# Optimization experiments

Hardware: AMD Instinct MI355X
Metric: run time of the kernel (lower is better)

## Reference

```python
import jax, jax.numpy as jnp
import numpy as np

B, T, C, I = 4, 4096, 1024, 4096

def rmsnorm(x, w, eps=1e-6):
    return x * jax.lax.rsqrt(jnp.mean(x * x, axis=-1, keepdims=True) + eps) * w

def shift(h):
    # prepend zeros, drop last timestep: (B,T,C)
    return jnp.pad(h, ((0, 0), (1, 0), (0, 0)))[:, :-1]

def wkv_scan(k, v, w, u):
    # k, v: (B,T,C) fp32; w, u: (C,)
    ew = jnp.exp(jnp.clip(w, -20.0, 20.0))
    def step(carry, kv):
        a, b = carry
        kt, vt = kv  # (B,C)
        ekt = jnp.exp(jnp.clip(u + kt, -20.0, 20.0))
        out = (a + ekt * vt) / (b + ekt + 1e-8)
        ek = jnp.exp(jnp.clip(kt, -20.0, 20.0))
        return (ew * a + ek * vt, ew * b + ek), out
    init = (jnp.zeros((k.shape[0], k.shape[2]), jnp.float32),
            jnp.zeros((k.shape[0], k.shape[2]), jnp.float32))
    _, out = jax.lax.scan(step, init, (k.swapaxes(0, 1), v.swapaxes(0, 1)))
    return out.swapaxes(0, 1)  # (B,T,C)

def setup_inputs() -> dict:
    key = jax.random.key(0)
    ks = jax.random.split(key, 16)
    s = 1.0 / np.sqrt(C)
    si = 1.0 / np.sqrt(I)
    return {
        "x": jax.random.normal(ks[0], (B, T, C), jnp.float32),
        "ln1_w": jnp.ones((C,), jnp.float32),
        "ln2_w": jnp.ones((C,), jnp.float32),
        "time_decay": jax.random.normal(ks[1], (C,), jnp.float32) * 0.1 - 5.0,
        "time_first": jax.random.normal(ks[2], (C,), jnp.float32) * 0.01,
        "time_mix_k": jnp.full((C,), 0.5, jnp.float32),
        "time_mix_v": jnp.full((C,), 0.5, jnp.float32),
        "time_mix_r": jnp.full((C,), 0.5, jnp.float32),
        "W_key": jax.random.normal(ks[3], (C, C), jnp.float32) * s,
        "W_value": jax.random.normal(ks[4], (C, C), jnp.float32) * s,
        "W_recept": jax.random.normal(ks[5], (C, C), jnp.float32) * s,
        "W_out": jax.random.normal(ks[6], (C, C), jnp.float32) * s,
        "time_mix_k2": jnp.full((C,), 0.5, jnp.float32),
        "time_mix_r2": jnp.full((C,), 0.5, jnp.float32),
        "W_key2": jax.random.normal(ks[7], (C, I), jnp.float32) * s,
        "W_value2": jax.random.normal(ks[8], (I, C), jnp.float32) * si,
        "W_recept2": jax.random.normal(ks[9], (C, C), jnp.float32) * s,
    }

def reference(x, ln1_w, ln2_w, time_decay, time_first,
              time_mix_k, time_mix_v, time_mix_r,
              W_key, W_value, W_recept, W_out,
              time_mix_k2, time_mix_r2, W_key2, W_value2, W_recept2):
    # --- time mixing ---
    h = rmsnorm(x, ln1_w)
    sh = shift(h)
    xk = h * time_mix_k + sh * (1 - time_mix_k)
    xv = h * time_mix_v + sh * (1 - time_mix_v)
    xr = h * time_mix_r + sh * (1 - time_mix_r)
    k = xk @ W_key
    v = xv @ W_value
    r = jax.nn.sigmoid(xr @ W_recept)
    w = -jnp.exp(time_decay)
    u = time_first
    wkv = wkv_scan(k.astype(jnp.float32), v.astype(jnp.float32), w, u).astype(x.dtype)
    x = x + (r * wkv) @ W_out
    # --- channel mixing ---
    h = rmsnorm(x, ln2_w)
    sh = shift(h)
    xk = h * time_mix_k2 + sh * (1 - time_mix_k2)
    xr = h * time_mix_r2 + sh * (1 - time_mix_r2)
    k2 = jnp.square(jax.nn.relu(xk @ W_key2))
    r2 = jax.nn.sigmoid(xr @ W_recept2)
    return x + r2 * (k2 @ W_value2)
```

## Files before the change

### kernel.cpp

```cpp
#include <hip/hip_runtime.h>
#include <cstdint>
#include <cstddef>

#define B_ 4
#define T_ 4096
#define C_ 1024
#define I_ 4096
#define M_ (B_*T_)

__device__ __forceinline__ float bf2f(uint16_t u) {
    union { uint32_t i; float f; } v; v.i = ((uint32_t)u) << 16; return v.f;
}
__device__ __forceinline__ uint16_t f2bf(float f) {
    union { float f; uint32_t i; } v; v.f = f;
    uint32_t i = v.i;
    return (uint16_t)((i + 0x7fffu + ((i >> 16) & 1u)) >> 16);
}

typedef __bf16 bf16x8 __attribute__((ext_vector_type(8)));
typedef float  f32x4  __attribute__((ext_vector_type(4)));

__device__ __forceinline__ void async16(const void* g, void* l) {
    __builtin_amdgcn_global_load_lds(
        (const __attribute__((address_space(1))) void*)g,
        (__attribute__((address_space(3))) void*)l, 16, 0, 0);
}

__global__ void sniff_kernel(const uint32_t* __restrict__ w,
                             int* __restrict__ flag, int* __restrict__ one) {
    *flag = (w[0] == 0x3F003F00u) ? 1 : 0;
    *one = 1;
}

struct VecPtrs { const void* s[9]; uint16_t* d[9]; };
__global__ __launch_bounds__(256) void convert_vecs(VecPtrs p, const int* __restrict__ flagp) {
    const int f = *flagp;
    const int tid = threadIdx.x;
    for (int a = 0; a < 9; ++a) {
        const void* s = p.s[a]; uint16_t* d = p.d[a];
        for (int i = tid; i < C_; i += 256)
            d[i] = f ? ((const uint16_t*)s)[i] : f2bf(((const float*)s)[i]);
    }
}

struct TJobs { const void* src[7]; uint16_t* dst[7]; };
__global__ __launch_bounds__(256) void transpose_all(TJobs tj, const int* __restrict__ flagp)
{
    __shared__ uint16_t tile[64][65];
    const int f = *flagp;
    const int bid = blockIdx.x;
    int w, t, R, Cc, cx, cy;
    if (bid < 1280) {
        w = bid >> 8; t = bid & 255; R = C_; Cc = C_; cx = t & 15; cy = t >> 4;
    } else if (bid < 2304) {
        w = 5; t = bid - 1280; R = C_; Cc = I_; cx = t & 63; cy = t >> 6;
    } else {
        w = 6; t = bid - 2304; R = I_; Cc = C_; cx = t & 15; cy = t >> 4;
    }
    const void* in = tj.src[w];
    uint16_t* out = tj.dst[w];
    const int lc = threadIdx.x & 63;
    const int rg = threadIdx.x >> 6;
    const int c0 = cx * 64, r0 = cy * 64;
    #pragma unroll
    for (int i = 0; i < 16; ++i) {
        int lr = rg * 16 + i;
        size_t idx = (size_t)(r0 + lr) * Cc + c0 + lc;
        tile[lr][lc] = f ? ((const uint16_t*)in)[idx] : f2bf(((const float*)in)[idx]);
    }
    __syncthreads();
    #pragma unroll
    for (int i = 0; i < 16; ++i) {
        int lcc = rg * 16 + i;
        out[(size_t)(c0 + lcc) * R + r0 + lc] = tile[lc][lcc];
    }
}

__global__ __launch_bounds__(256) void mix_kernel(
    const void* __restrict__ x, const uint16_t* __restrict__ ln,
    const uint16_t* __restrict__ mk, const uint16_t* __restrict__ mv,
    const uint16_t* __restrict__ mr, const int* __restrict__ flagp,
    uint16_t* __restrict__ xk, uint16_t* __restrict__ xv, uint16_t* __restrict__ xr)
{
    const int row = blockIdx.x;
    const int tid = threadIdx.x;
    const int f = *flagp;
    const bool hasPrev = (row & (T_ - 1)) != 0;
    const size_t base = (size_t)row * C_;

    float c[4], p[4];
    if (f) {
        const uint16_t* xb = (const uint16_t*)x;
        uint2 cu = ((const uint2*)(xb + base))[tid];
        uint2 pu; pu.x = 0u; pu.y = 0u;
        if (hasPrev) pu = ((const uint2*)(xb + base - C_))[tid];
        c[0] = bf2f((uint16_t)(cu.x & 0xffff)); c[1] = bf2f((uint16_t)(cu.x >> 16));
        c[2] = bf2f((uint16_t)(cu.y & 0xffff)); c[3] = bf2f((uint16_t)(cu.y >> 16));
        p[0] = bf2f((uint16_t)(pu.x & 0xffff)); p[1] = bf2f((uint16_t)(pu.x >> 16));
        p[2] = bf2f((uint16_t)(pu.y & 0xffff)); p[3] = bf2f((uint16_t)(pu.y >> 16));
    } else {
        const float* xf = (const float*)x;
        float4 cf = ((const float4*)(xf + base))[tid];
        float4 pf; pf.x = pf.y = pf.z = pf.w = 0.f;
        if (hasPrev) pf = ((const float4*)(xf + base - C_))[tid];
        c[0] = cf.x; c[1] = cf.y; c[2] = cf.z; c[3] = cf.w;
        p[0] = pf.x; p[1] = pf.y; p[2] = pf.z; p[3] = pf.w;
    }

    float s1 = c[0]*c[0] + c[1]*c[1] + c[2]*c[2] + c[3]*c[3];
    float s2 = p[0]*p[0] + p[1]*p[1] + p[2]*p[2] + p[3]*p[3];
    #pragma unroll
    for (int off = 32; off > 0; off >>= 1) {
        s1 += __shfl_down(s1, off);
        s2 += __shfl_down(s2, off);
    }
    __shared__ float red[8];
    const int lane = tid & 63, wave = tid >> 6;
    if (lane == 0) { red[wave * 2] = s1; red[wave * 2 + 1] = s2; }
    __syncthreads();
    s1 = red[0] + red[2] + red[4] + red[6];
    s2 = red[1] + red[3] + red[5] + red[7];
    const float rs1 = rsqrtf(s1 * (1.f / C_) + 1e-6f);
    const float rs2 = rsqrtf(s2 * (1.f / C_) + 1e-6f);

    uint2 lnu = ((const uint2*)ln)[tid];
    uint2 mku = ((const uint2*)mk)[tid];
    uint2 mru = ((const uint2*)mr)[tid];
    float lnv[4] = { bf2f((uint16_t)(lnu.x & 0xffff)), bf2f((uint16_t)(lnu.x >> 16)),
                     bf2f((uint16_t)(lnu.y & 0xffff)), bf2f((uint16_t)(lnu.y >> 16)) };
    float mkv[4] = { bf2f((uint16_t)(mku.x & 0xffff)), bf2f((uint16_t)(mku.x >> 16)),
                     bf2f((uint16_t)(mku.y & 0xffff)), bf2f((uint16_t)(mku.y >> 16)) };
    float mrv[4] = { bf2f((uint16_t)(mru.x & 0xffff)), bf2f((uint16_t)(mru.x >> 16)),
                     bf2f((uint16_t)(mru.y & 0xffff)), bf2f((uint16_t)(mru.y >> 16)) };

    float h[4], sh[4];
    #pragma unroll
    for (int e = 0; e < 4; ++e) {
        h[e]  = c[e] * rs1 * lnv[e];
        sh[e] = p[e] * rs2 * lnv[e];
    }

    uint16_t ok[4], orr[4];
    #pragma unroll
    for (int e = 0; e < 4; ++e) {
        ok[e]  = f2bf(h[e] * mkv[e] + sh[e] * (1.f - mkv[e]));
        orr[e] = f2bf(h[e] * mrv[e] + sh[e] * (1.f - mrv[e]));
    }
    uint2 w;
    w.x = (uint32_t)ok[0] | ((uint32_t)ok[1] << 16);  w.y = (uint32_t)ok[2] | ((uint32_t)ok[3] << 16);
    ((uint2*)(xk + base))[tid] = w;
    w.x = (uint32_t)orr[0] | ((uint32_t)orr[1] << 16); w.y = (uint32_t)orr[2] | ((uint32_t)orr[3] << 16);
    ((uint2*)(xr + base))[tid] = w;

    if (xv != nullptr) {
        uint2 mvu = ((const uint2*)mv)[tid];
        float mvv[4] = { bf2f((uint16_t)(mvu.x & 0xffff)), bf2f((uint16_t)(mvu.x >> 16)),
                         bf2f((uint16_t)(mvu.y & 0xffff)), bf2f((uint16_t)(mvu.y >> 16)) };
        uint16_t ov[4];
        #pragma unroll
        for (int e = 0; e < 4; ++e)
            ov[e] = f2bf(h[e] * mvv[e] + sh[e] * (1.f - mvv[e]));
        w.x = (uint32_t)ov[0] | ((uint32_t)ov[1] << 16);  w.y = (uint32_t)ov[2] | ((uint32_t)ov[3] << 16);
        ((uint2*)(xv + base))[tid] = w;
    }
}

#define SCAN_L   64
#define SCAN_NCH (T_ / SCAN_L)

__global__ __launch_bounds__(256) void wkv_pass1(
    const uint16_t* __restrict__ kb, const uint16_t* __restrict__ vb,
    const uint16_t* __restrict__ td,
    float* __restrict__ sumA, float* __restrict__ sumB)
{
    const int gid = blockIdx.x * 256 + threadIdx.x;
    const int c = gid & (C_ - 1);
    const int j = (gid >> 10) & (SCAN_NCH - 1);
    const int b = gid >> 16;
    float w = -__expf(bf2f(td[c]));
    w = fminf(fmaxf(w, -20.f), 20.f);
    const float ew = __expf(w);
    const size_t base = ((size_t)(b * T_ + j * SCAN_L)) * C_ + c;
    float A = 0.f, Bs = 0.f;
    #pragma unroll 8
    for (int i = 0; i < SCAN_L; ++i) {
        float kt = bf2f(kb[base + (size_t)i * C_]);
        float vt = bf2f(vb[base + (size_t)i * C_]);
        float ek = __expf(fminf(fmaxf(kt, -20.f), 20.f));
        A  = ew * A  + ek * vt;
        Bs = ew * Bs + ek;
    }
    const size_t sidx = ((size_t)(b * SCAN_NCH + j)) * C_ + c;
    sumA[sidx] = A; sumB[sidx] = Bs;
}

__global__ __launch_bounds__(256) void wkv_pass2(
    const float* __restrict__ sumA, const float* __restrict__ sumB,
    const uint16_t* __restrict__ td,
    float* __restrict__ a0s, float* __restrict__ b0s)
{
    const int gid = blockIdx.x * 256 + threadIdx.x;
    const int c = gid & (C_ - 1);
    const int b = gid >> 10;
    float w = -__expf(bf2f(td[c]));
    w = fminf(fmaxf(w, -20.f), 20.f);
    const float dL = __expf(w * (float)SCAN_L);
    float a = 0.f, bs = 0.f;
    for (int j = 0; j < SCAN_NCH; ++j) {
        size_t idx = ((size_t)(b * SCAN_NCH + j)) * C_ + c;
        a0s[idx] = a; b0s[idx] = bs;
        a  = dL * a  + sumA[idx];
        bs = dL * bs + sumB[idx];
    }
}

__global__ __launch_bounds__(256) void wkv_pass3(
    const uint16_t* __restrict__ kb, const uint16_t* __restrict__ vb,
    const uint16_t* __restrict__ rb, const uint16_t* __restrict__ td,
    const uint16_t* __restrict__ tf,
    const float* __restrict__ a0s, const float* __restrict__ b0s,
    uint16_t* __restrict__ rwkv)
{
    const int gid = blockIdx.x * 256 + threadIdx.x;
    const int c = gid & (C_ - 1);
    const int j = (gid >> 10) & (SCAN_NCH - 1);
    const int b = gid >> 16;
    float w = -__expf(bf2f(td[c]));
    w = fminf(fmaxf(w, -20.f), 20.f);
    const float ew = __expf(w);
    const float u = bf2f(tf[c]);
    const size_t base = ((size_t)(b * T_ + j * SCAN_L)) * C_ + c;
    const size_t sidx = ((size_t)(b * SCAN_NCH + j)) * C_ + c;
    float a = a0s[sidx], bs = b0s[sidx];
    #pragma unroll 4
    for (int i = 0; i < SCAN_L; ++i) {
        float kt = bf2f(kb[base + (size_t)i * C_]);
        float vt = bf2f(vb[base + (size_t)i * C_]);
        float rt = bf2f(rb[base + (size_t)i * C_]);
        float eu = __expf(fminf(fmaxf(u + kt, -20.f), 20.f));
        float out = __fdividef(a + eu * vt, bs + eu + 1e-8f);
        rwkv[base + (size_t)i * C_] = f2bf(rt * out);
        float ek = __expf(fminf(fmaxf(kt, -20.f), 20.f));
        a  = ew * a  + ek * vt;
        bs = ew * bs + ek;
    }
}

struct GJob {
    const uint16_t* A; const uint16_t* BT; void* Out;
    const void* aux1;
    int mode; int N; int K;
};
struct GJobs { GJob j[3]; };

#define EP_PITCH 72
#define EP_QUAD  4608

__global__ __launch_bounds__(256) void gemm_rt(GJobs js, const int* __restrict__ flagp)
{
    __shared__ uint16_t smem[18432];
    uint16_t* sA = smem;
    uint16_t* sB = smem + 8192;

    const GJob jb = js.j[blockIdx.z];
    const int N = jb.N, K = jb.K, mode = jb.mode;
    const int tid = threadIdx.x;
    const int lane = tid & 63, wave = tid >> 6;
    const int wr = wave >> 1, wc = wave & 1;
    const int laneM = lane & 15, quad = lane >> 4;

    const int pid = blockIdx.y * gridDim.x + blockIdx.x;
    const int group_size = 16 * gridDim.x;
    const int grp = pid / group_size;
    const int sub = pid - grp * group_size;
    const int pm = grp * 16 + (sub & 15);
    const int pn = sub >> 4;
    if (pn * 128 >= N) return;
    const int tileM = pm * 128, tileN = pn * 128;

    int f = 1;
    if (mode == 2) f = *flagp;

    f32x4 acc[4][4];
    #pragma unroll
    for (int i = 0; i < 4; ++i)
        #pragma unroll
        for (int j = 0; j < 4; ++j)
            acc[i][j] = (f32x4){0.f, 0.f, 0.f, 0.f};

    const uint16_t* Abase = jb.A  + (size_t)tileM * K;
    const uint16_t* Bbase = jb.BT + (size_t)tileN * K;

    int srow[4], scol[4];
    #pragma unroll
    for (int it = 0; it < 4; ++it) {
        int g = it * 256 + tid;
        srow[it] = g >> 3;
        scol[it] = ((g & 7) ^ (srow[it] & 7)) * 8;
    }
    const int swz = laneM & 7;

    for (int kt = 0; kt < K; kt += 64) {
        #pragma unroll
        for (int it = 0; it < 4; ++it)
            async16(Abase + (size_t)srow[it] * K + kt + scol[it], &sA[(it * 256 + tid) * 8]);
        #pragma unroll
        for (int it = 0; it < 4; ++it)
            async16(Bbase + (size_t)srow[it] * K + kt + scol[it], &sB[(it * 256 + tid) * 8]);
        __syncthreads();
        #pragma unroll
        for (int h = 0; h < 2; ++h) {
            bf16x8 av[4], bv[4];
            const int gk = (h * 4 + quad) ^ swz;
            #pragma unroll
            for (int i = 0; i < 4; ++i) {
                av[i] = *(const bf16x8*)&sA[(wr * 64 + i * 16 + laneM) * 64 + gk * 8];
                bv[i] = *(const bf16x8*)&sB[(wc * 64 + i * 16 + laneM) * 64 + gk * 8];
            }
            #pragma unroll
            for (int i = 0; i < 4; ++i)
                #pragma unroll
                for (int j = 0; j < 4; ++j)
                    acc[i][j] = __builtin_amdgcn_mfma_f32_16x16x32_bf16(av[i], bv[j], acc[i][j], 0, 0, 0);
        }
        __syncthreads();
    }

    const int qbase = (wr * 2 + wc) * EP_QUAD;
    #pragma unroll
    for (int i = 0; i < 4; ++i) {
        #pragma unroll
        for (int j = 0; j < 4; ++j) {
            #pragma unroll
            for (int rr = 0; rr < 4; ++rr) {
                float v = acc[i][j][rr];
                if (mode == 1) v = __fdividef(1.f, 1.f + __expf(-v));
                else if (mode == 3) { float t = fmaxf(v, 0.f); v = t * t; }
                smem[qbase + (i * 16 + quad * 4 + rr) * EP_PITCH + j * 16 + laneM] = f2bf(v);
            }
        }
    }
    __syncthreads();

    #pragma unroll
    for (int s = 0; s < 8; ++s) {
        int segid = s * 256 + tid;
        int gr = segid >> 4;
        int c0 = (segid & 15) * 8;
        int lidx = ((gr >> 6) * 2 + (c0 >> 6)) * EP_QUAD + (gr & 63) * EP_PITCH + (c0 & 63);
        uint4 pk = *(const uint4*)&smem[lidx];
        size_t idx = (size_t)(tileM + gr) * N + tileN + c0;

        if (mode != 2) {
            *(uint4*)((uint16_t*)jb.Out + idx) = pk;
        } else {
            union { uint4 u; uint16_t h[8]; } P; P.u = pk;
            float xres[8];
            if (f) {
                union { uint4 u; uint16_t h[8]; } A1;
                A1.u = *(const uint4*)((const uint16_t*)jb.aux1 + idx);
                #pragma unroll
                for (int e = 0; e < 8; ++e) xres[e] = bf2f(A1.h[e]);
            } else {
                const float* af = (const float*)jb.aux1 + idx;
                float4 a0 = *(const float4*)af;
                float4 a1 = *(const float4*)(af + 4);
                xres[0]=a0.x; xres[1]=a0.y; xres[2]=a0.z; xres[3]=a0.w;
                xres[4]=a1.x; xres[5]=a1.y; xres[6]=a1.z; xres[7]=a1.w;
            }
            union { uint4 u; uint16_t h[8]; } O;
            #pragma unroll
            for (int e = 0; e < 8; ++e) O.h[e] = f2bf(bf2f(P.h[e]) + xres[e]);
            *(uint4*)((uint16_t*)jb.Out + idx) = O.u;
        }
    }
}

__global__ __launch_bounds__(256) void gemm_fused(
    const uint16_t* __restrict__ Ar, const uint16_t* __restrict__ BTr, int K2,
    const uint16_t* __restrict__ Ak, const uint16_t* __restrict__ BTk, int K,
    const uint16_t* __restrict__ x2, void* __restrict__ Out,
    const int* __restrict__ flagp)
{
    __shared__ uint16_t smem[18432];
    uint16_t* sA = smem;
    uint16_t* sB = smem + 8192;

    const int N = C_;
    const int tid = threadIdx.x;
    const int lane = tid & 63, wave = tid >> 6;
    const int wr = wave >> 1, wc = wave & 1;
    const int laneM = lane & 15, quad = lane >> 4;

    const int pid = blockIdx.y * gridDim.x + blockIdx.x;
    const int group_size = 16 * gridDim.x;
    const int grp = pid / group_size;
    const int sub = pid - grp * group_size;
    const int pm = grp * 16 + (sub & 15);
    const int pn = sub >> 4;
    const int tileM = pm * 128, tileN = pn * 128;

    const int f = *flagp;

    int srow[4], scol[4];
    #pragma unroll
    for (int it = 0; it < 4; ++it) {
        int g = it * 256 + tid;
        srow[it] = g >> 3;
        scol[it] = ((g & 7) ^ (srow[it] & 7)) * 8;
    }
    const int swz = laneM & 7;

    f32x4 acc[4][4];
    #pragma unroll
    for (int i = 0; i < 4; ++i)
        #pragma unroll
        for (int j = 0; j < 4; ++j)
            acc[i][j] = (f32x4){0.f, 0.f, 0.f, 0.f};

    {
        const uint16_t* Abase = Ar  + (size_t)tileM * K2;
        const uint16_t* Bbase = BTr + (size_t)tileN * K2;
        for (int kt = 0; kt < K2; kt += 64) {
            #pragma unroll
            for (int it = 0; it < 4; ++it)
                async16(Abase + (size_t)srow[it] * K2 + kt + scol[it], &sA[(it * 256 + tid) * 8]);
            #pragma unroll
            for (int it = 0; it < 4; ++it)
                async16(Bbase + (size_t)srow[it] * K2 + kt + scol[it], &sB[(it * 256 + tid) * 8]);
            __syncthreads();
            #pragma unroll
            for (int h = 0; h < 2; ++h) {
                bf16x8 av[4], bv[4];
                const int gk = (h * 4 + quad) ^ swz;
                #pragma unroll
                for (int i = 0; i < 4; ++i) {
                    av[i] = *(const bf16x8*)&sA[(wr * 64 + i * 16 + laneM) * 64 + gk * 8];
                    bv[i] = *(const bf16x8*)&sB[(wc * 64 + i * 16 + laneM) * 64 + gk * 8];
                }
                #pragma unroll
                for (int i = 0; i < 4; ++i)
                    #pragma unroll
                    for (int j = 0; j < 4; ++j)
                        acc[i][j] = __builtin_amdgcn_mfma_f32_16x16x32_bf16(av[i], bv[j], acc[i][j], 0, 0, 0);
            }
            __syncthreads();
        }
    }

    uint32_t r2p[4][4][2];
    #pragma unroll
    for (int i = 0; i < 4; ++i)
        #pragma unroll
        for (int j = 0; j < 4; ++j) {
            uint16_t h0 = f2bf(__fdividef(1.f, 1.f + __expf(-acc[i][j][0])));
            uint16_t h1 = f2bf(__fdividef(1.f, 1.f + __expf(-acc[i][j][1])));
            uint16_t h2 = f2bf(__fdividef(1.f, 1.f + __expf(-acc[i][j][2])));
            uint16_t h3 = f2bf(__fdividef(1.f, 1.f + __expf(-acc[i][j][3])));
            r2p[i][j][0] = (uint32_t)h0 | ((uint32_t)h1 << 16);
            r2p[i][j][1] = (uint32_t)h2 | ((uint32_t)h3 << 16);
            acc[i][j] = (f32x4){0.f, 0.f, 0.f, 0.f};
        }

    {
        const uint16_t* Abase = Ak  + (size_t)tileM * K;
        const uint16_t* Bbase = BTk + (size_t)tileN * K;
        for (int kt = 0; kt < K; kt += 64) {
            #pragma unroll
            for (int it = 0; it < 4; ++it)
                async16(Abase + (size_t)srow[it] * K + kt + scol[it], &sA[(it * 256 + tid) * 8]);
            #pragma unroll
            for (int it = 0; it < 4; ++it)
                async16(Bbase + (size_t)srow[it] * K + kt + scol[it], &sB[(it * 256 + tid) * 8]);
            __syncthreads();
            #pragma unroll
            for (int h = 0; h < 2; ++h) {
                bf16x8 av[4], bv[4];
                const int gk = (h * 4 + quad) ^ swz;
                #pragma unroll
                for (int i = 0; i < 4; ++i) {
                    av[i] = *(const bf16x8*)&sA[(wr * 64 + i * 16 + laneM) * 64 + gk * 8];
                    bv[i] = *(const bf16x8*)&sB[(wc * 64 + i * 16 + laneM) * 64 + gk * 8];
                }
                #pragma unroll
                for (int i = 0; i < 4; ++i)
                    #pragma unroll
                    for (int j = 0; j < 4; ++j)
                        acc[i][j] = __builtin_amdgcn_mfma_f32_16x16x32_bf16(av[i], bv[j], acc[i][j], 0, 0, 0);
            }
            __syncthreads();
        }
    }

    const int qbase = (wr * 2 + wc) * EP_QUAD;
    #pragma unroll
    for (int i = 0; i < 4; ++i) {
        #pragma unroll
        for (int j = 0; j < 4; ++j) {
            #pragma unroll
            for (int rr = 0; rr < 4; ++rr) {
                uint16_t rh = (uint16_t)(r2p[i][j][rr >> 1] >> ((rr & 1) * 16));
                float v = bf2f(rh) * acc[i][j][rr];
                smem[qbase + (i * 16 + quad * 4 + rr) * EP_PITCH + j * 16 + laneM] = f2bf(v);
            }
        }
    }
    __syncthreads();

    #pragma unroll
    for (int s = 0; s < 8; ++s) {
        int segid = s * 256 + tid;
        int gr = segid >> 4;
        int c0 = (segid & 15) * 8;
        int lidx = ((gr >> 6) * 2 + (c0 >> 6)) * EP_QUAD + (gr & 63) * EP_PITCH + (c0 & 63);
        union { uint4 u; uint16_t h[8]; } P;
        P.u = *(const uint4*)&smem[lidx];
        size_t idx = (size_t)(tileM + gr) * N + tileN + c0;
        union { uint4 u; uint16_t h[8]; } X;
        X.u = *(const uint4*)(x2 + idx);
        float res[8];
        #pragma unroll
        for (int e = 0; e < 8; ++e) res[e] = bf2f(X.h[e]) + bf2f(P.h[e]);
        if (f) {
            union { uint4 u; uint16_t h[8]; } O;
            #pragma unroll
            for (int e = 0; e < 8; ++e) O.h[e] = f2bf(res[e]);
            *(uint4*)((uint16_t*)Out + idx) = O.u;
        } else {
            float* of = (float*)Out + idx;
            *(float4*)of       = (float4){res[0], res[1], res[2], res[3]};
            *(float4*)(of + 4) = (float4){res[4], res[5], res[6], res[7]};
        }
    }
}

extern "C" void kernel_launch(void* const* d_in, const int* in_sizes, int n_in,
                              void* d_out, int out_size, void* d_ws, size_t ws_size,
                              hipStream_t stream)
{
    const void* x   = d_in[0];
    const void* ln1 = d_in[1];
    const void* ln2 = d_in[2];
    const void* td  = d_in[3];
    const void* tf  = d_in[4];
    const void* mk  = d_in[5];
    const void* mv  = d_in[6];
    const void* mr  = d_in[7];
    const void* Wk  = d_in[8];
    const void* Wv  = d_in[9];
    const void* Wr  = d_in[10];
    const void* Wo  = d_in[11];
    const void* mk2 = d_in[12];
    const void* mr2 = d_in[13];
    const void* Wk2 = d_in[14];
    const void* Wv2 = d_in[15];
    const void* Wr2 = d_in[16];

    char* ws = (char*)d_ws;
    const size_t MiB = 1u << 20;
    uint16_t* WkT  = (uint16_t*)(ws + 0 * MiB);
    uint16_t* WvT  = (uint16_t*)(ws + 2 * MiB);
    uint16_t* WrT  = (uint16_t*)(ws + 4 * MiB);
    uint16_t* WoT  = (uint16_t*)(ws + 6 * MiB);
    uint16_t* Wr2T = (uint16_t*)(ws + 8 * MiB);
    uint16_t* Wk2T = (uint16_t*)(ws + 10 * MiB);
    uint16_t* Wv2T = (uint16_t*)(ws + 18 * MiB);
    uint16_t* A0 = (uint16_t*)(ws + 26 * MiB);
    uint16_t* A1 = (uint16_t*)(ws + 58 * MiB);
    uint16_t* A2 = (uint16_t*)(ws + 90 * MiB);
    uint16_t* A3 = (uint16_t*)(ws + 122 * MiB);
    uint16_t* A4 = (uint16_t*)(ws + 154 * MiB);
    uint16_t* A5 = (uint16_t*)(ws + 186 * MiB);
    uint16_t* k2 = (uint16_t*)(ws + 122 * MiB);
    float* sumA = (float*)(ws + 58 * MiB);
    float* sumB = (float*)(ws + 59 * MiB);
    float* a0s  = (float*)(ws + 60 * MiB);
    float* b0s  = (float*)(ws + 61 * MiB);
    int* flagp = (int*)(ws + 250 * MiB);
    int* onep  = (int*)(ws + 250 * MiB + 16);
    uint16_t* vecs = (uint16_t*)(ws + 250 * MiB + 64);
    uint16_t* ln1c = vecs + 0 * C_;
    uint16_t* ln2c = vecs + 1 * C_;
    uint16_t* tdc  = vecs + 2 * C_;
    uint16_t* tfc  = vecs + 3 * C_;
    uint16_t* mkc  = vecs + 4 * C_;
    uint16_t* mvc  = vecs + 5 * C_;
    uint16_t* mrc  = vecs + 6 * C_;
    uint16_t* mk2c = vecs + 7 * C_;
    uint16_t* mr2c = vecs + 8 * C_;

    uint16_t* xk   = A0;
    uint16_t* xv   = A1;
    uint16_t* xr   = A2;
    uint16_t* kb   = A3;
    uint16_t* vb   = A4;
    uint16_t* rb   = A5;
    uint16_t* rwkv = A0;
    uint16_t* x2   = A1;
    uint16_t* xk2  = A2;
    uint16_t* xr2  = A0;

    dim3 blk(256);

    sniff_kernel<<<1, 1, 0, stream>>>((const uint32_t*)mk, flagp, onep);
    VecPtrs vp;
    vp.s[0] = ln1; vp.s[1] = ln2; vp.s[2] = td;  vp.s[3] = tf;  vp.s[4] = mk;
    vp.s[5] = mv;  vp.s[6] = mr;  vp.s[7] = mk2; vp.s[8] = mr2;
    vp.d[0] = ln1c; vp.d[1] = ln2c; vp.d[2] = tdc;  vp.d[3] = tfc;  vp.d[4] = mkc;
    vp.d[5] = mvc;  vp.d[6] = mrc;  vp.d[7] = mk2c; vp.d[8] = mr2c;
    convert_vecs<<<1, blk, 0, stream>>>(vp, flagp);

    TJobs tj;
    tj.src[0] = Wk;  tj.dst[0] = WkT;
    tj.src[1] = Wv;  tj.dst[1] = WvT;
    tj.src[2] = Wr;  tj.dst[2] = WrT;
    tj.src[3] = Wo;  tj.dst[3] = WoT;
    tj.src[4] = Wr2; tj.dst[4] = Wr2T;
    tj.src[5] = Wk2; tj.dst[5] = Wk2T;
    tj.src[6] = Wv2; tj.dst[6] = Wv2T;
    transpose_all<<<3328, blk, 0, stream>>>(tj, flagp);

    mix_kernel<<<M_, blk, 0, stream>>>(x, ln1c, mkc, mvc, mrc, flagp, xk, xv, xr);

    GJobs kvr;
    kvr.j[0] = GJob{ xk, WkT, kb, nullptr, 0, C_, C_ };
    kvr.j[1] = GJob{ xv, WvT, vb, nullptr, 0, C_, C_ };
    kvr.j[2] = GJob{ xr, WrT, rb, nullptr, 1, C_, C_ };
    gemm_rt<<<dim3(C_ / 128, M_ / 128, 3), blk, 0, stream>>>(kvr, flagp);

    wkv_pass1<<<(B_ * SCAN_NCH * C_) / 256, blk, 0, stream>>>(kb, vb, tdc, sumA, sumB);
    wkv_pass2<<<(B_ * C_) / 256, blk, 0, stream>>>(sumA, sumB, tdc, a0s, b0s);
    wkv_pass3<<<(B_ * SCAN_NCH * C_) / 256, blk, 0, stream>>>(kb, vb, rb, tdc, tfc, a0s, b0s, rwkv);

    GJobs g2; g2.j[0] = GJob{ rwkv, WoT, x2, x, 2, C_, C_ };
    g2.j[1] = g2.j[0]; g2.j[2] = g2.j[0];
    gemm_rt<<<dim3(C_ / 128, M_ / 128, 1), blk, 0, stream>>>(g2, flagp);

    mix_kernel<<<M_, blk, 0, stream>>>(x2, ln2c, mk2c, nullptr, mr2c, onep, xk2, nullptr, xr2);

    GJobs g3; g3.j[0] = GJob{ xk2, Wk2T, k2, nullptr, 3, I_, C_ };
    g3.j[1] = g3.j[0]; g3.j[2] = g3.j[0];
    gemm_rt<<<dim3(I_ / 128, M_ / 128, 1), blk, 0, stream>>>(g3, flagp);

    gemm_fused<<<dim3(C_ / 128, M_ / 128), blk, 0, stream>>>(
        xr2, Wr2T, C_, k2, Wv2T, I_, x2, d_out, flagp);

    (void)in_sizes; (void)n_in; (void)out_size; (void)ws_size;
}
```

Measured before the change: 952.0 us.

## Replace 128x128 GEMMs with double-buffered 256x256 tile GEMM and split fused FFN GEMM

Replaces the 128x128-tile, 256-thread GEMM kernels with a 256x256-tile, 512-thread kernel. It double-buffers LDS through async global-to-LDS loads, interleaves half-tile MFMA phases with barriers and raised wave priority, and uses a grouped tile ordering. The fused receptance+value GEMM is split into two launches: a sigmoid GEMM that writes r2 to a buffer, and a K=4096 GEMM whose epilogue computes x + r*P. The aim is higher arithmetic intensity and overlap of memory loads with MFMA work, at the cost of more LDS and registers per block and an extra round trip of r2 through memory.

```diff
diff --git a/kernel.cpp b/kernel.cpp
--- a/kernel.cpp
+++ b/kernel.cpp
@@ -25,6 +25,9 @@
         (const __attribute__((address_space(1))) void*)g,
         (__attribute__((address_space(3))) void*)l, 16, 0, 0);
 }
+
+#define MEMBAR asm volatile("" ::: "memory")
+#define BAR    __builtin_amdgcn_s_barrier()
 
 __global__ void sniff_kernel(const uint32_t* __restrict__ w,
                              int* __restrict__ flag, int* __restrict__ one) {
@@ -246,9 +249,10 @@
     }
 }
 
+
 struct GJob {
     const uint16_t* A; const uint16_t* BT; void* Out;
-    const void* aux1;
+    const void* aux1; const void* aux2;
     int mode; int N; int K;
 };
 struct GJobs { GJob j[3]; };
@@ -256,280 +260,201 @@
 #define EP_PITCH 72
 #define EP_QUAD  4608
 
-__global__ __launch_bounds__(256) void gemm_rt(GJobs js, const int* __restrict__ flagp)
-{
-    __shared__ uint16_t smem[18432];
+#define MFMA_QUAD(RB)                                                         \
+    _Pragma("unroll")                                                         \
+    for (int ii = 0; ii < 4; ++ii) {                                          \
+        _Pragma("unroll")                                                     \
+        for (int jj = 0; jj < 4; ++jj)                                        \
+            acc[(RB) + ii][jj] = __builtin_amdgcn_mfma_f32_16x16x32_bf16(     \
+                av[ii], bv[jj], acc[(RB) + ii][jj], 0, 0, 0);                 \
+    }
+
+__device__ __forceinline__ void gemm_loop256(
+    const uint16_t* __restrict__ Abase, const uint16_t* __restrict__ Bbase,
+    const int K, uint16_t* __restrict__ sA, uint16_t* __restrict__ sB,
+    const int tid, const int aOff, const int bOff, f32x4 (&acc)[8][4])
+{
+    const int r0  = tid >> 2;
+    const int kg8 = ((tid & 3) ^ (r0 & 3)) * 8;
+    const uint16_t* gA = Abase + (size_t)r0 * K + kg8;
+    const uint16_t* gB = Bbase + (size_t)r0 * K + kg8;
+    uint16_t* dA = sA + tid * 8;
+    uint16_t* dB = sB + tid * 8;
+    const size_t qs = (size_t)128 * K;
+    const int NT = K >> 6;
+
+    async16(gA,      dA);         async16(gA + qs,      dA + 4096);
+    async16(gB,      dB);         async16(gB + qs,      dB + 4096);
+    async16(gA + 32, dA + 8192);  async16(gA + 32 + qs, dA + 12288);
+    async16(gB + 32, dB + 8192);  async16(gB + 32 + qs, dB + 12288);
+    asm volatile("s_waitcnt vmcnt(4)" ::: "memory");
+    BAR; MEMBAR;
+
+    for (int t = 0; t < NT; ++t) {
+        const int s0 = (t & 1) * 2;
+        const int n0 = s0 ^ 2;
+        const uint16_t* A0 = sA + s0 * 8192 + aOff;
+        const uint16_t* B0 = sB + s0 * 8192 + bOff;
+        const uint16_t* A1 = A0 + 8192;
+        const uint16_t* B1 = B0 + 8192;
+        uint16_t* dAn = dA + n0 * 8192;
+        uint16_t* dBn = dB + n0 * 8192;
+        const bool pf = (t + 1 < NT);
+        const int ko = (t + 1) << 6;
+        bf16x8 av[4], bv[4];
+
+        #pragma unroll
+        for (int ii = 0; ii < 4; ++ii) av[ii] = *(const bf16x8*)(A0 + ii * 512);
+        #pragma unroll
+        for (int jj = 0; jj < 4; ++jj) bv[jj] = *(const bf16x8*)(B0 + jj * 512);
+        if (pf) { async16(gA + ko, dAn); async16(gA + ko + qs, dAn + 4096); }
+        MEMBAR;
+        BAR; MEMBAR;
+        __builtin_amdgcn_s_setprio(1);
+        MFMA_QUAD(0)
+        __builtin_amdgcn_s_setprio(0);
+        BAR; MEMBAR;
+
+        #pragma unroll
+        for (int ii = 0; ii < 4; ++ii) av[ii] = *(const bf16x8*)(A0 + 2048 + ii * 512);
+        if (pf) { async16(gB + ko, dBn); async16(gB + ko + qs, dBn + 4096); }
+        if (pf) asm volatile("s_waitcnt vmcnt(4)" ::: "memory");
+        else    asm volatile("s_waitcnt vmcnt(0)" ::: "memory");
+        BAR; MEMBAR;
+        __builtin_amdgcn_s_setprio(1);
+        MFMA_QUAD(4)
+        __builtin_amdgcn_s_setprio(0);
+        BAR; MEMBAR;
+
+        #pragma unroll
+        for (int ii = 0; ii < 4; ++ii) av[ii] = *(const bf16x8*)(A1 + ii * 512);
+        #pragma unroll
+        for (int jj = 0; jj < 4; ++jj) bv[jj] = *(const bf16x8*)(B1 + jj * 512);
+        if (pf) { async16(gA + ko + 32, dAn + 8192); async16(gA + ko + 32 + qs, dAn + 12288); }
+        MEMBAR;
+        BAR; MEMBAR;
+        __builtin_amdgcn_s_setprio(1);
+        MFMA_QUAD(0)
+        __builtin_amdgcn_s_setprio(0);
+        BAR; MEMBAR;
+
+        #pragma unroll
+        for (int ii = 0; ii < 4; ++ii) av[ii] = *(const bf16x8*)(A1 + 2048 + ii * 512);
+        if (pf) { async16(gB + ko + 32, dBn + 8192); async16(gB + ko + 32 + qs, dBn + 12288); }
+        if (pf) asm volatile("s_waitcnt vmcnt(4)" ::: "memory");
+        BAR; MEMBAR;
+        __builtin_amdgcn_s_setprio(1);
+        MFMA_QUAD(4)
+        __builtin_amdgcn_s_setprio(0);
+        BAR; MEMBAR;
+    }
+}
+
+__global__ __launch_bounds__(512, 2) void gemm256(GJobs js, const int* __restrict__ flagp)
+{
+    __shared__ uint16_t smem[65536];
     uint16_t* sA = smem;
-    uint16_t* sB = smem + 8192;
+    uint16_t* sB = smem + 32768;
 
     const GJob jb = js.j[blockIdx.z];
     const int N = jb.N, K = jb.K, mode = jb.mode;
     const int tid = threadIdx.x;
     const int lane = tid & 63, wave = tid >> 6;
-    const int wr = wave >> 1, wc = wave & 1;
     const int laneM = lane & 15, quad = lane >> 4;
-
-    const int pid = blockIdx.y * gridDim.x + blockIdx.x;
-    const int group_size = 16 * gridDim.x;
-    const int grp = pid / group_size;
-    const int sub = pid - grp * group_size;
-    const int pm = grp * 16 + (sub & 15);
-    const int pn = sub >> 4;
-    if (pn * 128 >= N) return;
-    const int tileM = pm * 128, tileN = pn * 128;
-
-    int f = 1;
-    if (mode == 2) f = *flagp;
-
-    f32x4 acc[4][4];
-    #pragma unroll
-    for (int i = 0; i < 4; ++i)
+    const int wm = wave >> 2, wn = wave & 3;
+
+    const int nwg = gridDim.x;
+    const int pid = blockIdx.x;
+    const int spid = (pid & 7) * (nwg >> 3) + (pid >> 3);
+    const int pm = spid & 63;
+    const int pn = spid >> 6;
+    const int tileM = pm << 8, tileN = pn << 8;
+
+    const int slot8 = (quad ^ (laneM & 3)) * 8;
+    const int aOff = (wm * 128 + laneM) * 32 + slot8;
+    const int bOff = (wn * 64  + laneM) * 32 + slot8;
+
+    f32x4 acc[8][4];
+    #pragma unroll
+    for (int i = 0; i < 8; ++i)
         #pragma unroll
         for (int j = 0; j < 4; ++j)
             acc[i][j] = (f32x4){0.f, 0.f, 0.f, 0.f};
 
-    const uint16_t* Abase = jb.A  + (size_t)tileM * K;
-    const uint16_t* Bbase = jb.BT + (size_t)tileN * K;
-
-    int srow[4], scol[4];
-    #pragma unroll
-    for (int it = 0; it < 4; ++it) {
-        int g = it * 256 + tid;
-        srow[it] = g >> 3;
-        scol[it] = ((g & 7) ^ (srow[it] & 7)) * 8;
-    }
-    const int swz = laneM & 7;
-
-    for (int kt = 0; kt < K; kt += 64) {
-        #pragma unroll
-        for (int it = 0; it < 4; ++it)
-            async16(Abase + (size_t)srow[it] * K + kt + scol[it], &sA[(it * 256 + tid) * 8]);
-        #pragma unroll
-        for (int it = 0; it < 4; ++it)
-            async16(Bbase + (size_t)srow[it] * K + kt + scol[it], &sB[(it * 256 + tid) * 8]);
-        __syncthreads();
-        #pragma unroll
-        for (int h = 0; h < 2; ++h) {
-            bf16x8 av[4], bv[4];
-            const int gk = (h * 4 + quad) ^ swz;
+    gemm_loop256(jb.A + (size_t)tileM * K, jb.BT + (size_t)tileN * K,
+                 K, sA, sB, tid, aOff, bOff, acc);
+
+    const int f = (mode == 2 || mode == 4) ? *flagp : 1;
+
+    #pragma unroll
+    for (int h = 0; h < 2; ++h) {
+        if (h) __syncthreads();
+        #pragma unroll
+        for (int ii = 0; ii < 4; ++ii) {
             #pragma unroll
-            for (int i = 0; i < 4; ++i) {
-                av[i] = *(const bf16x8*)&sA[(wr * 64 + i * 16 + laneM) * 64 + gk * 8];
-                bv[i] = *(const bf16x8*)&sB[(wc * 64 + i * 16 + laneM) * 64 + gk * 8];
+            for (int jj = 0; jj < 4; ++jj) {
+                #pragma unroll
+                for (int rr = 0; rr < 4; ++rr) {
+                    float v = acc[h * 4 + ii][jj][rr];
+                    if (mode == 1) v = __fdividef(1.f, 1.f + __expf(-v));
+                    else if (mode == 3) { float tt = fmaxf(v, 0.f); v = tt * tt; }
+                    smem[wave * EP_QUAD + (ii * 16 + quad * 4 + rr) * EP_PITCH
+                         + jj * 16 + laneM] = f2bf(v);
+                }
             }
-            #pragma unroll
-            for (int i = 0; i < 4; ++i)
-                #pragma unroll
-                for (int j = 0; j < 4; ++j)
-                    acc[i][j] = __builtin_amdgcn_mfma_f32_16x16x32_bf16(av[i], bv[j], acc[i][j], 0, 0, 0);
         }
         __syncthreads();
-    }
-
-    const int qbase = (wr * 2 + wc) * EP_QUAD;
-    #pragma unroll
-    for (int i = 0; i < 4; ++i) {
-        #pragma unroll
-        for (int j = 0; j < 4; ++j) {
-            #pragma unroll
-            for (int rr = 0; rr < 4; ++rr) {
-                float v = acc[i][j][rr];
-                if (mode == 1) v = __fdividef(1.f, 1.f + __expf(-v));
-                else if (mode == 3) { float t = fmaxf(v, 0.f); v = t * t; }
-                smem[qbase + (i * 16 + quad * 4 + rr) * EP_PITCH + j * 16 + laneM] = f2bf(v);
+        #pragma unroll
+        for (int s = 0; s < 8; ++s) {
+            int segid = s * 512 + tid;
+            int gr = segid >> 5;
+            int c0 = (segid & 31) * 8;
+            int band = gr >> 6, lr = gr & 63;
+            int lidx = (band * 4 + (c0 >> 6)) * EP_QUAD + lr * EP_PITCH + (c0 & 63);
+            uint4 pk = *(const uint4*)&smem[lidx];
+            size_t idx = (size_t)(tileM + band * 128 + h * 64 + lr) * N + tileN + c0;
+
+            if (mode == 2) {
+                union { uint4 u; uint16_t hh[8]; } P; P.u = pk;
+                float xres[8];
+                if (f) {
+                    union { uint4 u; uint16_t hh[8]; } A1u;
+                    A1u.u = *(const uint4*)((const uint16_t*)jb.aux1 + idx);
+                    #pragma unroll
+                    for (int e = 0; e < 8; ++e) xres[e] = bf2f(A1u.hh[e]);
+                } else {
+                    const float* af = (const float*)jb.aux1 + idx;
+                    float4 a0 = *(const float4*)af;
+                    float4 a1 = *(const float4*)(af + 4);
+                    xres[0]=a0.x; xres[1]=a0.y; xres[2]=a0.z; xres[3]=a0.w;
+                    xres[4]=a1.x; xres[5]=a1.y; xres[6]=a1.z; xres[7]=a1.w;
+                }
+                union { uint4 u; uint16_t hh[8]; } O;
+                #pragma unroll
+                for (int e = 0; e < 8; ++e) O.hh[e] = f2bf(bf2f(P.hh[e]) + xres[e]);
+                *(uint4*)((uint16_t*)jb.Out + idx) = O.u;
+            } else if (mode == 4) {
+                union { uint4 u; uint16_t hh[8]; } P, X, R;
+                P.u = pk;
+                X.u = *(const uint4*)((const uint16_t*)jb.aux1 + idx);
+                R.u = *(const uint4*)((const uint16_t*)jb.aux2 + idx);
+                float res[8];
+                #pragma unroll
+                for (int e = 0; e < 8; ++e)
+                    res[e] = bf2f(X.hh[e]) + bf2f(R.hh[e]) * bf2f(P.hh[e]);
+                if (f) {
+                    union { uint4 u; uint16_t hh[8]; } O;
+                    #pragma unroll
+                    for (int e = 0; e < 8; ++e) O.hh[e] = f2bf(res[e]);
+                    *(uint4*)((uint16_t*)jb.Out + idx) = O.u;
+                } else {
+                    float* of = (float*)jb.Out + idx;
+                    *(float4*)of       = (float4){res[0], res[1], res[2], res[3]};
+                    *(float4*)(of + 4) = (float4){res[4], res[5], res[6], res[7]};
+                }
+            } else {
+                *(uint4*)((uint16_t*)jb.Out + idx) = pk;
             }
-        }
-    }
-    __syncthreads();
-
-    #pragma unroll
-    for (int s = 0; s < 8; ++s) {
-        int segid = s * 256 + tid;
-        int gr = segid >> 4;
-        int c0 = (segid & 15) * 8;
-        int lidx = ((gr >> 6) * 2 + (c0 >> 6)) * EP_QUAD + (gr & 63) * EP_PITCH + (c0 & 63);
-        uint4 pk = *(const uint4*)&smem[lidx];
-        size_t idx = (size_t)(tileM + gr) * N + tileN + c0;
-
-        if (mode != 2) {
-            *(uint4*)((uint16_t*)jb.Out + idx) = pk;
-        } else {
-            union { uint4 u; uint16_t h[8]; } P; P.u = pk;
-            float xres[8];
-            if (f) {
-                union { uint4 u; uint16_t h[8]; } A1;
-                A1.u = *(const uint4*)((const uint16_t*)jb.aux1 + idx);
-                #pragma unroll
-                for (int e = 0; e < 8; ++e) xres[e] = bf2f(A1.h[e]);
-            } else {
-                const float* af = (const float*)jb.aux1 + idx;
-                float4 a0 = *(const float4*)af;
-                float4 a1 = *(const float4*)(af + 4);
-                xres[0]=a0.x; xres[1]=a0.y; xres[2]=a0.z; xres[3]=a0.w;
-                xres[4]=a1.x; xres[5]=a1.y; xres[6]=a1.z; xres[7]=a1.w;
-            }
-            union { uint4 u; uint16_t h[8]; } O;
-            #pragma unroll
-            for (int e = 0; e < 8; ++e) O.h[e] = f2bf(bf2f(P.h[e]) + xres[e]);
-            *(uint4*)((uint16_t*)jb.Out + idx) = O.u;
-        }
-    }
-}
-
-__global__ __launch_bounds__(256) void gemm_fused(
-    const uint16_t* __restrict__ Ar, const uint16_t* __restrict__ BTr, int K2,
-    const uint16_t* __restrict__ Ak, const uint16_t* __restrict__ BTk, int K,
-    const uint16_t* __restrict__ x2, void* __restrict__ Out,
-    const int* __restrict__ flagp)
-{
-    __shared__ uint16_t smem[18432];
-    uint16_t* sA = smem;
-    uint16_t* sB = smem + 8192;
-
-    const int N = C_;
-    const int tid = threadIdx.x;
-    const int lane = tid & 63, wave = tid >> 6;
-    const int wr = wave >> 1, wc = wave & 1;
-    const int laneM = lane & 15, quad = lane >> 4;
-
-    const int pid = blockIdx.y * gridDim.x + blockIdx.x;
-    const int group_size = 16 * gridDim.x;
-    const int grp = pid / group_size;
-    const int sub = pid - grp * group_size;
-    const int pm = grp * 16 + (sub & 15);
-    const int pn = sub >> 4;
-    const int tileM = pm * 128, tileN = pn * 128;
-
-    const int f = *flagp;
-
-    int srow[4], scol[4];
-    #pragma unroll
-    for (int it = 0; it < 4; ++it) {
-        int g = it * 256 + tid;
-        srow[it] = g >> 3;
-        scol[it] = ((g & 7) ^ (srow[it] & 7)) * 8;
-    }
-    const int swz = laneM & 7;
-
-    f32x4 acc[4][4];
-    #pragma unroll
-    for (int i = 0; i < 4; ++i)
-        #pragma unroll
-        for (int j = 0; j < 4; ++j)
-            acc[i][j] = (f32x4){0.f, 0.f, 0.f, 0.f};
-
-    {
-        const uint16_t* Abase = Ar  + (size_t)tileM * K2;
-        const uint16_t* Bbase = BTr + (size_t)tileN * K2;
-        for (int kt = 0; kt < K2; kt += 64) {
-            #pragma unroll
-            for (int it = 0; it < 4; ++it)
-                async16(Abase + (size_t)srow[it] * K2 + kt + scol[it], &sA[(it * 256 + tid) * 8]);
-            #pragma unroll
-            for (int it = 0; it < 4; ++it)
-                async16(Bbase + (size_t)srow[it] * K2 + kt + scol[it], &sB[(it * 256 + tid) * 8]);
-            __syncthreads();
-            #pragma unroll
-            for (int h = 0; h < 2; ++h) {
-                bf16x8 av[4], bv[4];
-                const int gk = (h * 4 + quad) ^ swz;
-                #pragma unroll
-                for (int i = 0; i < 4; ++i) {
-                    av[i] = *(const bf16x8*)&sA[(wr * 64 + i * 16 + laneM) * 64 + gk * 8];
-                    bv[i] = *(const bf16x8*)&sB[(wc * 64 + i * 16 + laneM) * 64 + gk * 8];
-                }
-                #pragma unroll
-                for (int i = 0; i < 4; ++i)
-                    #pragma unroll
-                    for (int j = 0; j < 4; ++j)
-                        acc[i][j] = __builtin_amdgcn_mfma_f32_16x16x32_bf16(av[i], bv[j], acc[i][j], 0, 0, 0);
-            }
-            __syncthreads();
-        }
-    }
-
-    uint32_t r2p[4][4][2];
-    #pragma unroll
-    for (int i = 0; i < 4; ++i)
-        #pragma unroll
-        for (int j = 0; j < 4; ++j) {
-            uint16_t h0 = f2bf(__fdividef(1.f, 1.f + __expf(-acc[i][j][0])));
-            uint16_t h1 = f2bf(__fdividef(1.f, 1.f + __expf(-acc[i][j][1])));
-            uint16_t h2 = f2bf(__fdividef(1.f, 1.f + __expf(-acc[i][j][2])));
-            uint16_t h3 = f2bf(__fdividef(1.f, 1.f + __expf(-acc[i][j][3])));
-            r2p[i][j][0] = (uint32_t)h0 | ((uint32_t)h1 << 16);
-            r2p[i][j][1] = (uint32_t)h2 | ((uint32_t)h3 << 16);
-            acc[i][j] = (f32x4){0.f, 0.f, 0.f, 0.f};
-        }
-
-    {
-        const uint16_t* Abase = Ak  + (size_t)tileM * K;
-        const uint16_t* Bbase = BTk + (size_t)tileN * K;
-        for (int kt = 0; kt < K; kt += 64) {
-            #pragma unroll
-            for (int it = 0; it < 4; ++it)
-                async16(Abase + (size_t)srow[it] * K + kt + scol[it], &sA[(it * 256 + tid) * 8]);
-            #pragma unroll
-            for (int it = 0; it < 4; ++it)
-                async16(Bbase + (size_t)srow[it] * K + kt + scol[it], &sB[(it * 256 + tid) * 8]);
-            __syncthreads();
-            #pragma unroll
-            for (int h = 0; h < 2; ++h) {
-                bf16x8 av[4], bv[4];
-                const int gk = (h * 4 + quad) ^ swz;
-                #pragma unroll
-                for (int i = 0; i < 4; ++i) {
-                    av[i] = *(const bf16x8*)&sA[(wr * 64 + i * 16 + laneM) * 64 + gk * 8];
-                    bv[i] = *(const bf16x8*)&sB[(wc * 64 + i * 16 + laneM) * 64 + gk * 8];
-                }
-                #pragma unroll
-                for (int i = 0; i < 4; ++i)
-                    #pragma unroll
-                    for (int j = 0; j < 4; ++j)
-                        acc[i][j] = __builtin_amdgcn_mfma_f32_16x16x32_bf16(av[i], bv[j], acc[i][j], 0, 0, 0);
-            }
-            __syncthreads();
-        }
-    }
-
-    const int qbase = (wr * 2 + wc) * EP_QUAD;
-    #pragma unroll
-    for (int i = 0; i < 4; ++i) {
-        #pragma unroll
-        for (int j = 0; j < 4; ++j) {
-            #pragma unroll
-            for (int rr = 0; rr < 4; ++rr) {
-                uint16_t rh = (uint16_t)(r2p[i][j][rr >> 1] >> ((rr & 1) * 16));
-                float v = bf2f(rh) * acc[i][j][rr];
-                smem[qbase + (i * 16 + quad * 4 + rr) * EP_PITCH + j * 16 + laneM] = f2bf(v);
-            }
-        }
-    }
-    __syncthreads();
-
-    #pragma unroll
-    for (int s = 0; s < 8; ++s) {
-        int segid = s * 256 + tid;
-        int gr = segid >> 4;
-        int c0 = (segid & 15) * 8;
-        int lidx = ((gr >> 6) * 2 + (c0 >> 6)) * EP_QUAD + (gr & 63) * EP_PITCH + (c0 & 63);
-        union { uint4 u; uint16_t h[8]; } P;
-        P.u = *(const uint4*)&smem[lidx];
-        size_t idx = (size_t)(tileM + gr) * N + tileN + c0;
-        union { uint4 u; uint16_t h[8]; } X;
-        X.u = *(const uint4*)(x2 + idx);
-        float res[8];
-        #pragma unroll
-        for (int e = 0; e < 8; ++e) res[e] = bf2f(X.h[e]) + bf2f(P.h[e]);
-        if (f) {
-            union { uint4 u; uint16_t h[8]; } O;
-            #pragma unroll
-            for (int e = 0; e < 8; ++e) O.h[e] = f2bf(res[e]);
-            *(uint4*)((uint16_t*)Out + idx) = O.u;
-        } else {
-            float* of = (float*)Out + idx;
-            *(float4*)of       = (float4){res[0], res[1], res[2], res[3]};
-            *(float4*)(of + 4) = (float4){res[4], res[5], res[6], res[7]};
         }
     }
 }
@@ -599,6 +524,7 @@
     uint16_t* x2   = A1;
     uint16_t* xk2  = A2;
     uint16_t* xr2  = A0;
+    uint16_t* r2   = A2;
 
     dim3 blk(256);
 
@@ -623,27 +549,32 @@
     mix_kernel<<<M_, blk, 0, stream>>>(x, ln1c, mkc, mvc, mrc, flagp, xk, xv, xr);
 
     GJobs kvr;
-    kvr.j[0] = GJob{ xk, WkT, kb, nullptr, 0, C_, C_ };
-    kvr.j[1] = GJob{ xv, WvT, vb, nullptr, 0, C_, C_ };
-    kvr.j[2] = GJob{ xr, WrT, rb, nullptr, 1, C_, C_ };
-    gemm_rt<<<dim3(C_ / 128, M_ / 128, 3), blk, 0, stream>>>(kvr, flagp);
+    kvr.j[0] = GJob{ xk, WkT, kb, nullptr, nullptr, 0, C_, C_ };
+    kvr.j[1] = GJob{ xv, WvT, vb, nullptr, nullptr, 0, C_, C_ };
+    kvr.j[2] = GJob{ xr, WrT, rb, nullptr, nullptr, 1, C_, C_ };
+    gemm256<<<dim3(64 * (C_ >> 8), 1, 3), 512, 0, stream>>>(kvr, flagp);
 
     wkv_pass1<<<(B_ * SCAN_NCH * C_) / 256, blk, 0, stream>>>(kb, vb, tdc, sumA, sumB);
     wkv_pass2<<<(B_ * C_) / 256, blk, 0, stream>>>(sumA, sumB, tdc, a0s, b0s);
     wkv_pass3<<<(B_ * SCAN_NCH * C_) / 256, blk, 0, stream>>>(kb, vb, rb, tdc, tfc, a0s, b0s, rwkv);
 
-    GJobs g2; g2.j[0] = GJob{ rwkv, WoT, x2, x, 2, C_, C_ };
+    GJobs g2; g2.j[0] = GJob{ rwkv, WoT, x2, x, nullptr, 2, C_, C_ };
     g2.j[1] = g2.j[0]; g2.j[2] = g2.j[0];
-    gemm_rt<<<dim3(C_ / 128, M_ / 128, 1), blk, 0, stream>>>(g2, flagp);
+    gemm256<<<dim3(64 * (C_ >> 8), 1, 1), 512, 0, stream>>>(g2, flagp);
 
     mix_kernel<<<M_, blk, 0, stream>>>(x2, ln2c, mk2c, nullptr, mr2c, onep, xk2, nullptr, xr2);
 
-    GJobs g3; g3.j[0] = GJob{ xk2, Wk2T, k2, nullptr, 3, I_, C_ };
+    GJobs g3; g3.j[0] = GJob{ xk2, Wk2T, k2, nullptr, nullptr, 3, I_, C_ };
     g3.j[1] = g3.j[0]; g3.j[2] = g3.j[0];
-    gemm_rt<<<dim3(I_ / 128, M_ / 128, 1), blk, 0, stream>>>(g3, flagp);
-
-    gemm_fused<<<dim3(C_ / 128, M_ / 128), blk, 0, stream>>>(
-        xr2, Wr2T, C_, k2, Wv2T, I_, x2, d_out, flagp);
+    gemm256<<<dim3(64 * (I_ >> 8), 1, 1), 512, 0, stream>>>(g3, flagp);
+
+    GJobs g4a; g4a.j[0] = GJob{ xr2, Wr2T, r2, nullptr, nullptr, 1, C_, C_ };
+    g4a.j[1] = g4a.j[0]; g4a.j[2] = g4a.j[0];
+    gemm256<<<dim3(64 * (C_ >> 8), 1, 1), 512, 0, stream>>>(g4a, flagp);
+
+    GJobs g4b; g4b.j[0] = GJob{ k2, Wv2T, d_out, x2, r2, 4, C_, I_ };
+    g4b.j[1] = g4b.j[0]; g4b.j[2] = g4b.j[0];
+    gemm256<<<dim3(64 * (C_ >> 8), 1, 1), 512, 0, stream>>>(g4b, flagp);
 
     (void)in_sizes; (void)n_in; (void)out_size; (void)ws_size;
 }
```

New measurement: 872.1 us. 8.4% less time.
